# Optimization experiments

Hardware: AMD Instinct MI355X
Metric: run time of the kernel (lower is better)

Reference implementation:

```python
import jax, jax.numpy as jnp
import numpy as np

B, T, D_IN, H, D_OUT = 4096, 512, 10, 20, 2


def setup_inputs() -> dict:
    key = jax.random.key(0)
    ks = jax.random.split(key, 12)
    s = 1.0 / np.sqrt(H)  # PyTorch-style uniform bound scale (use normal*s)
    return {
        "x": jax.random.normal(ks[0], (B, T, D_IN), jnp.float32),
        "w_ih0": jax.random.normal(ks[1], (H, D_IN), jnp.float32) * s,
        "w_hh0": jax.random.normal(ks[2], (H, H), jnp.float32) * s,
        "b_ih0": jax.random.normal(ks[3], (H,), jnp.float32) * s,
        "b_hh0": jax.random.normal(ks[4], (H,), jnp.float32) * s,
        "w_ih1": jax.random.normal(ks[5], (H, H), jnp.float32) * s,
        "w_hh1": jax.random.normal(ks[6], (H, H), jnp.float32) * s,
        "b_ih1": jax.random.normal(ks[7], (H,), jnp.float32) * s,
        "b_hh1": jax.random.normal(ks[8], (H,), jnp.float32) * s,
        "fc_w": jax.random.normal(ks[9], (D_OUT, H), jnp.float32) * s,
        "fc_b": jax.random.normal(ks[10], (D_OUT,), jnp.float32) * s,
    }


def _rnn_layer(inp, w_ih, w_hh, b_ih, b_hh):
    # inp: [B, T, Din]. Precompute input projection once (batched GEMM),
    # then scan the sequential recurrence: h_t = tanh(x_t W_ih^T + b_ih + h_{t-1} W_hh^T + b_hh)
    xp = jnp.einsum('btd,hd->bth', inp, w_ih) + (b_ih + b_hh)  # [B, T, H]

    def step(h, xt):
        h = jnp.tanh(xt + h @ w_hh.T)
        return h, h

    h0 = jnp.zeros((inp.shape[0], w_hh.shape[0]), inp.dtype)
    _, hs = jax.lax.scan(step, h0, jnp.swapaxes(xp, 0, 1))  # hs: [T, B, H]
    return jnp.swapaxes(hs, 0, 1)  # [B, T, H]


def reference(x, w_ih0, w_hh0, b_ih0, b_hh0, w_ih1, w_hh1, b_ih1, b_hh1, fc_w, fc_b):
    h1 = _rnn_layer(x, w_ih0, w_hh0, b_ih0, b_hh0)
    h2 = _rnn_layer(h1, w_ih1, w_hh1, b_ih1, b_hh1)
    last = h2[:, -1, :]  # [B, H]
    return last @ fc_w.T + fc_b  # [B, D_OUT]
```

## Files before the change

### kernel.cpp

```cpp
#include <hip/hip_runtime.h>
#include <cstdint>

constexpr int B_   = 4096;
constexpr int T_   = 512;
constexpr int DIN  = 10;
constexpr int H_   = 20;
constexpr int DOUT = 2;

constexpr int SPW = 3;
constexpr int CH  = 4;
constexpr int XV  = CH * DIN / 4;

#define CFENCE() asm volatile("" ::: "memory")

__device__ __forceinline__ float fast_tanh(float v) {
    float e = __builtin_amdgcn_exp2f(v * 2.885390082f);
    float r = __builtin_amdgcn_rcpf(e + 1.0f);
    return fmaf(-2.0f, r, 1.0f);
}

extern "C" __global__ void __launch_bounds__(64, 1)
rnn_skew(const float* __restrict__ x,
         const float* __restrict__ w_ih0, const float* __restrict__ w_hh0,
         const float* __restrict__ b_ih0, const float* __restrict__ b_hh0,
         const float* __restrict__ w_ih1, const float* __restrict__ w_hh1,
         const float* __restrict__ b_ih1, const float* __restrict__ b_hh1,
         const float* __restrict__ fc_w, const float* __restrict__ fc_b,
         float* __restrict__ out)
{
    const int lane = threadIdx.x;
    const int sl   = lane / H_;
    const int i    = lane - sl * H_;
    const int samp = blockIdx.x * SPW + sl;
    const int sc   = (samp < B_) ? samp : (B_ - 1);
    const int slc  = (sl < SPW) ? sl : SPW;

    __shared__ __align__(16) float h1s[SPW + 1][H_];
    __shared__ __align__(16) float h2s[SPW + 1][H_];

    float wi0[DIN];
    {
        const float2* p = reinterpret_cast<const float2*>(w_ih0 + i * DIN);
        #pragma unroll
        for (int k = 0; k < DIN / 2; ++k) {
            float2 v = p[k];
            wi0[2 * k] = v.x; wi0[2 * k + 1] = v.y;
        }
    }
    float wh0[H_], wi1[H_], wh1[H_];
    {
        const float4* p0 = reinterpret_cast<const float4*>(w_hh0 + i * H_);
        const float4* p1 = reinterpret_cast<const float4*>(w_ih1 + i * H_);
        const float4* p2 = reinterpret_cast<const float4*>(w_hh1 + i * H_);
        #pragma unroll
        for (int k = 0; k < H_ / 4; ++k) {
            float4 a = p0[k]; wh0[4*k]=a.x; wh0[4*k+1]=a.y; wh0[4*k+2]=a.z; wh0[4*k+3]=a.w;
            float4 b = p1[k]; wi1[4*k]=b.x; wi1[4*k+1]=b.y; wi1[4*k+2]=b.z; wi1[4*k+3]=b.w;
            float4 c = p2[k]; wh1[4*k]=c.x; wh1[4*k+1]=c.y; wh1[4*k+2]=c.z; wh1[4*k+3]=c.w;
        }
    }
    const float bias0 = b_ih0[i] + b_hh0[i];
    const float bias1 = b_ih1[i] + b_hh1[i];

    float4 h1q[H_ / 4], h2q[H_ / 4];
    #pragma unroll
    for (int k = 0; k < H_ / 4; ++k) {
        h1q[k] = make_float4(0.f, 0.f, 0.f, 0.f);
        h2q[k] = make_float4(0.f, 0.f, 0.f, 0.f);
    }

    const float4* xb = reinterpret_cast<const float4*>(x + (size_t)sc * (T_ * DIN));

    float4 xv[XV];
    #pragma unroll
    for (int k = 0; k < XV; ++k) xv[k] = xb[k];

    auto full_step = [&](float xpm) {
        float a0 = xpm, a1 = 0.f, a2 = 0.f, a3 = 0.f;
        float b0 = bias1, b1 = 0.f, b2 = 0.f, b3 = 0.f;
        #pragma unroll
        for (int k = 0; k < H_ / 4; ++k) {
            a0 = fmaf(h1q[k].x, wh0[4*k+0], a0);
            a1 = fmaf(h1q[k].y, wh0[4*k+1], a1);
            a2 = fmaf(h1q[k].z, wh0[4*k+2], a2);
            a3 = fmaf(h1q[k].w, wh0[4*k+3], a3);
            b0 = fmaf(h1q[k].x, wi1[4*k+0], b0);
            b1 = fmaf(h1q[k].y, wi1[4*k+1], b1);
            b2 = fmaf(h1q[k].z, wi1[4*k+2], b2);
            b3 = fmaf(h1q[k].w, wi1[4*k+3], b3);
        }
        #pragma unroll
        for (int k = 0; k < H_ / 4; ++k) {
            b0 = fmaf(h2q[k].x, wh1[4*k+0], b0);
            b1 = fmaf(h2q[k].y, wh1[4*k+1], b1);
            b2 = fmaf(h2q[k].z, wh1[4*k+2], b2);
            b3 = fmaf(h2q[k].w, wh1[4*k+3], b3);
        }
        float h1n = fast_tanh((a0 + a1) + (a2 + a3));
        float h2n = fast_tanh((b0 + b1) + (b2 + b3));
        CFENCE();
        h1s[slc][i] = h1n;
        h2s[slc][i] = h2n;
        CFENCE();
        #pragma unroll
        for (int k = 0; k < H_ / 4; ++k)
            h1q[k] = reinterpret_cast<const float4*>(&h1s[slc][0])[k];
        #pragma unroll
        for (int k = 0; k < H_ / 4; ++k)
            h2q[k] = reinterpret_cast<const float4*>(&h2s[slc][0])[k];
        CFENCE();
    };

    auto consume_xp = [&](float* xp) {
        #pragma unroll
        for (int m = 0; m < CH; ++m) xp[m] = bias0;
        #pragma unroll
        for (int k = 0; k < XV; ++k) {
            int idx = 4 * k;
            xp[(idx+0)/DIN] = fmaf(xv[k].x, wi0[(idx+0)%DIN], xp[(idx+0)/DIN]);
            xp[(idx+1)/DIN] = fmaf(xv[k].y, wi0[(idx+1)%DIN], xp[(idx+1)/DIN]);
            xp[(idx+2)/DIN] = fmaf(xv[k].z, wi0[(idx+2)%DIN], xp[(idx+2)/DIN]);
            xp[(idx+3)/DIN] = fmaf(xv[k].w, wi0[(idx+3)%DIN], xp[(idx+3)/DIN]);
        }
    };

    {
        float xp[CH];
        consume_xp(xp);
        #pragma unroll
        for (int k = 0; k < XV; ++k) xv[k] = xb[(CH * DIN) / 4 + k];

        float h1n = fast_tanh(xp[0]);
        CFENCE();
        h1s[slc][i] = h1n;
        CFENCE();
        #pragma unroll
        for (int k = 0; k < H_ / 4; ++k)
            h1q[k] = reinterpret_cast<const float4*>(&h1s[slc][0])[k];
        CFENCE();

        #pragma unroll
        for (int m = 1; m < CH; ++m) full_step(xp[m]);
    }

    for (int t0 = CH; t0 < T_; t0 += CH) {
        float xp[CH];
        consume_xp(xp);
        {
            const int t0n = (t0 + CH < T_) ? (t0 + CH) : 0;
            #pragma unroll
            for (int k = 0; k < XV; ++k) xv[k] = xb[(t0n * DIN) / 4 + k];
        }
        #pragma unroll
        for (int m = 0; m < CH; ++m) full_step(xp[m]);
    }

    {
        float b0 = bias1, b1 = 0.f, b2 = 0.f, b3 = 0.f;
        #pragma unroll
        for (int k = 0; k < H_ / 4; ++k) {
            b0 = fmaf(h1q[k].x, wi1[4*k+0], b0);
            b1 = fmaf(h1q[k].y, wi1[4*k+1], b1);
            b2 = fmaf(h1q[k].z, wi1[4*k+2], b2);
            b3 = fmaf(h1q[k].w, wi1[4*k+3], b3);
        }
        #pragma unroll
        for (int k = 0; k < H_ / 4; ++k) {
            b0 = fmaf(h2q[k].x, wh1[4*k+0], b0);
            b1 = fmaf(h2q[k].y, wh1[4*k+1], b1);
            b2 = fmaf(h2q[k].z, wh1[4*k+2], b2);
            b3 = fmaf(h2q[k].w, wh1[4*k+3], b3);
        }
        float h2n = fast_tanh((b0 + b1) + (b2 + b3));
        CFENCE();
        h2s[slc][i] = h2n;
        CFENCE();
        #pragma unroll
        for (int k = 0; k < H_ / 4; ++k)
            h2q[k] = reinterpret_cast<const float4*>(&h2s[slc][0])[k];
        CFENCE();
    }

    if (sl < SPW && samp < B_ && i < DOUT) {
        float hf[H_];
        #pragma unroll
        for (int k = 0; k < H_ / 4; ++k) {
            hf[4*k+0] = h2q[k].x; hf[4*k+1] = h2q[k].y;
            hf[4*k+2] = h2q[k].z; hf[4*k+3] = h2q[k].w;
        }
        float acc = fc_b[i];
        #pragma unroll
        for (int j = 0; j < H_; ++j) acc = fmaf(hf[j], fc_w[i * H_ + j], acc);
        out[samp * DOUT + i] = acc;
    }
}

extern "C" void kernel_launch(void* const* d_in, const int* in_sizes, int n_in,
                              void* d_out, int out_size, void* d_ws, size_t ws_size,
                              hipStream_t stream) {
    (void)in_sizes; (void)n_in; (void)d_ws; (void)ws_size; (void)out_size;
    const float* x     = (const float*)d_in[0];
    const float* w_ih0 = (const float*)d_in[1];
    const float* w_hh0 = (const float*)d_in[2];
    const float* b_ih0 = (const float*)d_in[3];
    const float* b_hh0 = (const float*)d_in[4];
    const float* w_ih1 = (const float*)d_in[5];
    const float* w_hh1 = (const float*)d_in[6];
    const float* b_ih1 = (const float*)d_in[7];
    const float* b_hh1 = (const float*)d_in[8];
    const float* fc_w  = (const float*)d_in[9];
    const float* fc_b  = (const float*)d_in[10];
    float* out = (float*)d_out;

    const int grid = (B_ + SPW - 1) / SPW;
    hipLaunchKernelGGL(rnn_skew, dim3(grid), dim3(64), 0, stream,
                       x, w_ih0, w_hh0, b_ih0, b_hh0,
                       w_ih1, w_hh1, b_ih1, b_hh1, fc_w, fc_b, out);
}
```

Before: 154.3 us.

## Interleave two independent sample chains per lane to hide recurrence latency

Each 64-lane block now maps 2 samples per lane group (2 groups of 20 lanes) and runs two independent recurrences per lane, interleaving their compute and LDS exchange. The goal is ILP that hides the serial FMA/tanh/LDS latency of one chain behind the other. In exchange, 40 of 64 lanes are active instead of 60, there are fewer blocks (1024 vs 1366), register pressure roughly doubles, and the x chunk drops from 4 to 2 timesteps.

After: 242.3 us. 1.57x slower.

```diff
diff --git a/kernel.cpp b/kernel.cpp
--- a/kernel.cpp
+++ b/kernel.cpp
@@ -7,8 +7,9 @@
 constexpr int H_   = 20;
 constexpr int DOUT = 2;
 
-constexpr int SPW = 3;
-constexpr int CH  = 4;
+constexpr int SPW = 2;
+constexpr int NCH = 2;
+constexpr int CH  = 2;
 constexpr int XV  = CH * DIN / 4;
 
 #define CFENCE() asm volatile("" ::: "memory")
@@ -20,7 +21,7 @@
 }
 
 extern "C" __global__ void __launch_bounds__(64, 1)
-rnn_skew(const float* __restrict__ x,
+rnn_dual(const float* __restrict__ x,
          const float* __restrict__ w_ih0, const float* __restrict__ w_hh0,
          const float* __restrict__ b_ih0, const float* __restrict__ b_hh0,
          const float* __restrict__ w_ih1, const float* __restrict__ w_hh1,
@@ -31,12 +32,16 @@
     const int lane = threadIdx.x;
     const int sl   = lane / H_;
     const int i    = lane - sl * H_;
-    const int samp = blockIdx.x * SPW + sl;
-    const int sc   = (samp < B_) ? samp : (B_ - 1);
-    const int slc  = (sl < SPW) ? sl : SPW;
-
-    __shared__ __align__(16) float h1s[SPW + 1][H_];
-    __shared__ __align__(16) float h2s[SPW + 1][H_];
+    const bool act = (sl < SPW);
+    const int sampA = blockIdx.x * (SPW * NCH) + sl;
+    const int sampB = sampA + SPW;
+    const int scA = act ? min(sampA, B_ - 1) : (B_ - 1);
+    const int scB = act ? min(sampB, B_ - 1) : (B_ - 1);
+    const int rowA = act ? sl : 4;
+    const int rowB = act ? (SPW + sl) : 4;
+
+    __shared__ __align__(16) float h1s[2 * SPW + 1][H_];
+    __shared__ __align__(16) float h2s[2 * SPW + 1][H_];
 
     float wi0[DIN];
     {
@@ -62,20 +67,22 @@
     const float bias0 = b_ih0[i] + b_hh0[i];
     const float bias1 = b_ih1[i] + b_hh1[i];
 
-    float4 h1q[H_ / 4], h2q[H_ / 4];
+    float4 h1qA[H_/4], h2qA[H_/4], h1qB[H_/4], h2qB[H_/4];
     #pragma unroll
     for (int k = 0; k < H_ / 4; ++k) {
-        h1q[k] = make_float4(0.f, 0.f, 0.f, 0.f);
-        h2q[k] = make_float4(0.f, 0.f, 0.f, 0.f);
-    }
-
-    const float4* xb = reinterpret_cast<const float4*>(x + (size_t)sc * (T_ * DIN));
-
-    float4 xv[XV];
+        h1qA[k] = make_float4(0.f,0.f,0.f,0.f); h2qA[k] = make_float4(0.f,0.f,0.f,0.f);
+        h1qB[k] = make_float4(0.f,0.f,0.f,0.f); h2qB[k] = make_float4(0.f,0.f,0.f,0.f);
+    }
+
+    const float4* xbA = reinterpret_cast<const float4*>(x + (size_t)scA * (T_ * DIN));
+    const float4* xbB = reinterpret_cast<const float4*>(x + (size_t)scB * (T_ * DIN));
+
+    float4 xvA[XV], xvB[XV];
     #pragma unroll
-    for (int k = 0; k < XV; ++k) xv[k] = xb[k];
-
-    auto full_step = [&](float xpm) {
+    for (int k = 0; k < XV; ++k) { xvA[k] = xbA[k]; xvB[k] = xbB[k]; }
+
+    auto compute2 = [&](const float4 (&h1q)[H_/4], const float4 (&h2q)[H_/4],
+                        float xpm, float& h1n, float& h2n) {
         float a0 = xpm, a1 = 0.f, a2 = 0.f, a3 = 0.f;
         float b0 = bias1, b1 = 0.f, b2 = 0.f, b3 = 0.f;
         #pragma unroll
@@ -96,22 +103,36 @@
             b2 = fmaf(h2q[k].z, wh1[4*k+2], b2);
             b3 = fmaf(h2q[k].w, wh1[4*k+3], b3);
         }
-        float h1n = fast_tanh((a0 + a1) + (a2 + a3));
-        float h2n = fast_tanh((b0 + b1) + (b2 + b3));
-        CFENCE();
-        h1s[slc][i] = h1n;
-        h2s[slc][i] = h2n;
-        CFENCE();
+        h1n = fast_tanh((a0 + a1) + (a2 + a3));
+        h2n = fast_tanh((b0 + b1) + (b2 + b3));
+    };
+
+    auto readback = [&](float4 (&h1q)[H_/4], float4 (&h2q)[H_/4], int row) {
         #pragma unroll
         for (int k = 0; k < H_ / 4; ++k)
-            h1q[k] = reinterpret_cast<const float4*>(&h1s[slc][0])[k];
+            h1q[k] = reinterpret_cast<const float4*>(&h1s[row][0])[k];
         #pragma unroll
         for (int k = 0; k < H_ / 4; ++k)
-            h2q[k] = reinterpret_cast<const float4*>(&h2s[slc][0])[k];
-        CFENCE();
-    };
-
-    auto consume_xp = [&](float* xp) {
+            h2q[k] = reinterpret_cast<const float4*>(&h2s[row][0])[k];
+    };
+
+    auto step_pair = [&](float xpa, float xpb) {
+        float h1nA, h2nA, h1nB, h2nB;
+        compute2(h1qA, h2qA, xpa, h1nA, h2nA);
+        CFENCE();
+        h1s[rowA][i] = h1nA; h2s[rowA][i] = h2nA;
+        CFENCE();
+        compute2(h1qB, h2qB, xpb, h1nB, h2nB);
+        CFENCE();
+        h1s[rowB][i] = h1nB; h2s[rowB][i] = h2nB;
+        CFENCE();
+        readback(h1qA, h2qA, rowA);
+        CFENCE();
+        readback(h1qB, h2qB, rowB);
+        CFENCE();
+    };
+
+    auto consume_xp = [&](const float4 (&xv)[XV], float (&xp)[CH]) {
         #pragma unroll
         for (int m = 0; m < CH; ++m) xp[m] = bias0;
         #pragma unroll
@@ -125,73 +146,90 @@
     };
 
     {
-        float xp[CH];
-        consume_xp(xp);
-        #pragma unroll
-        for (int k = 0; k < XV; ++k) xv[k] = xb[(CH * DIN) / 4 + k];
-
-        float h1n = fast_tanh(xp[0]);
-        CFENCE();
-        h1s[slc][i] = h1n;
-        CFENCE();
-        #pragma unroll
-        for (int k = 0; k < H_ / 4; ++k)
-            h1q[k] = reinterpret_cast<const float4*>(&h1s[slc][0])[k];
-        CFENCE();
-
-        #pragma unroll
-        for (int m = 1; m < CH; ++m) full_step(xp[m]);
+        float xpA[CH], xpB[CH];
+        consume_xp(xvA, xpA);
+        consume_xp(xvB, xpB);
+        #pragma unroll
+        for (int k = 0; k < XV; ++k) {
+            xvA[k] = xbA[(CH * DIN) / 4 + k];
+            xvB[k] = xbB[(CH * DIN) / 4 + k];
+        }
+        float h1nA = fast_tanh(xpA[0]);
+        float h1nB = fast_tanh(xpB[0]);
+        CFENCE();
+        h1s[rowA][i] = h1nA; h1s[rowB][i] = h1nB;
+        CFENCE();
+        #pragma unroll
+        for (int k = 0; k < H_ / 4; ++k) {
+            h1qA[k] = reinterpret_cast<const float4*>(&h1s[rowA][0])[k];
+            h1qB[k] = reinterpret_cast<const float4*>(&h1s[rowB][0])[k];
+        }
+        CFENCE();
+        #pragma unroll
+        for (int m = 1; m < CH; ++m) step_pair(xpA[m], xpB[m]);
     }
 
     for (int t0 = CH; t0 < T_; t0 += CH) {
-        float xp[CH];
-        consume_xp(xp);
+        float xpA[CH], xpB[CH];
+        consume_xp(xvA, xpA);
+        consume_xp(xvB, xpB);
         {
             const int t0n = (t0 + CH < T_) ? (t0 + CH) : 0;
+            const int base = t0n * DIN / 4;
             #pragma unroll
-            for (int k = 0; k < XV; ++k) xv[k] = xb[(t0n * DIN) / 4 + k];
-        }
-        #pragma unroll
-        for (int m = 0; m < CH; ++m) full_step(xp[m]);
-    }
-
-    {
-        float b0 = bias1, b1 = 0.f, b2 = 0.f, b3 = 0.f;
-        #pragma unroll
-        for (int k = 0; k < H_ / 4; ++k) {
-            b0 = fmaf(h1q[k].x, wi1[4*k+0], b0);
-            b1 = fmaf(h1q[k].y, wi1[4*k+1], b1);
-            b2 = fmaf(h1q[k].z, wi1[4*k+2], b2);
-            b3 = fmaf(h1q[k].w, wi1[4*k+3], b3);
-        }
-        #pragma unroll
-        for (int k = 0; k < H_ / 4; ++k) {
-            b0 = fmaf(h2q[k].x, wh1[4*k+0], b0);
-            b1 = fmaf(h2q[k].y, wh1[4*k+1], b1);
-            b2 = fmaf(h2q[k].z, wh1[4*k+2], b2);
-            b3 = fmaf(h2q[k].w, wh1[4*k+3], b3);
-        }
-        float h2n = fast_tanh((b0 + b1) + (b2 + b3));
-        CFENCE();
-        h2s[slc][i] = h2n;
-        CFENCE();
-        #pragma unroll
-        for (int k = 0; k < H_ / 4; ++k)
-            h2q[k] = reinterpret_cast<const float4*>(&h2s[slc][0])[k];
-        CFENCE();
-    }
-
-    if (sl < SPW && samp < B_ && i < DOUT) {
-        float hf[H_];
-        #pragma unroll
-        for (int k = 0; k < H_ / 4; ++k) {
-            hf[4*k+0] = h2q[k].x; hf[4*k+1] = h2q[k].y;
-            hf[4*k+2] = h2q[k].z; hf[4*k+3] = h2q[k].w;
-        }
-        float acc = fc_b[i];
-        #pragma unroll
-        for (int j = 0; j < H_; ++j) acc = fmaf(hf[j], fc_w[i * H_ + j], acc);
-        out[samp * DOUT + i] = acc;
+            for (int k = 0; k < XV; ++k) { xvA[k] = xbA[base + k]; xvB[k] = xbB[base + k]; }
+        }
+        #pragma unroll
+        for (int m = 0; m < CH; ++m) step_pair(xpA[m], xpB[m]);
+    }
+
+    {
+        auto fin = [&](const float4 (&h1q)[H_/4], const float4 (&h2q)[H_/4]) -> float {
+            float b0 = bias1, b1 = 0.f, b2 = 0.f, b3 = 0.f;
+            #pragma unroll
+            for (int k = 0; k < H_ / 4; ++k) {
+                b0 = fmaf(h1q[k].x, wi1[4*k+0], b0);
+                b1 = fmaf(h1q[k].y, wi1[4*k+1], b1);
+                b2 = fmaf(h1q[k].z, wi1[4*k+2], b2);
+                b3 = fmaf(h1q[k].w, wi1[4*k+3], b3);
+            }
+            #pragma unroll
+            for (int k = 0; k < H_ / 4; ++k) {
+                b0 = fmaf(h2q[k].x, wh1[4*k+0], b0);
+                b1 = fmaf(h2q[k].y, wh1[4*k+1], b1);
+                b2 = fmaf(h2q[k].z, wh1[4*k+2], b2);
+                b3 = fmaf(h2q[k].w, wh1[4*k+3], b3);
+            }
+            return fast_tanh((b0 + b1) + (b2 + b3));
+        };
+        float h2nA = fin(h1qA, h2qA);
+        float h2nB = fin(h1qB, h2qB);
+        CFENCE();
+        h2s[rowA][i] = h2nA; h2s[rowB][i] = h2nB;
+        CFENCE();
+        #pragma unroll
+        for (int k = 0; k < H_ / 4; ++k) {
+            h2qA[k] = reinterpret_cast<const float4*>(&h2s[rowA][0])[k];
+            h2qB[k] = reinterpret_cast<const float4*>(&h2s[rowB][0])[k];
+        }
+        CFENCE();
+    }
+
+    if (act && i < DOUT) {
+        float accA = fc_b[i], accB = fc_b[i];
+        #pragma unroll
+        for (int k = 0; k < H_ / 4; ++k) {
+            accA = fmaf(h2qA[k].x, fc_w[i*H_ + 4*k+0], accA);
+            accA = fmaf(h2qA[k].y, fc_w[i*H_ + 4*k+1], accA);
+            accA = fmaf(h2qA[k].z, fc_w[i*H_ + 4*k+2], accA);
+            accA = fmaf(h2qA[k].w, fc_w[i*H_ + 4*k+3], accA);
+            accB = fmaf(h2qB[k].x, fc_w[i*H_ + 4*k+0], accB);
+            accB = fmaf(h2qB[k].y, fc_w[i*H_ + 4*k+1], accB);
+            accB = fmaf(h2qB[k].z, fc_w[i*H_ + 4*k+2], accB);
+            accB = fmaf(h2qB[k].w, fc_w[i*H_ + 4*k+3], accB);
+        }
+        if (sampA < B_) out[sampA * DOUT + i] = accA;
+        if (sampB < B_) out[sampB * DOUT + i] = accB;
     }
 }
 
@@ -212,8 +250,8 @@
     const float* fc_b  = (const float*)d_in[10];
     float* out = (float*)d_out;
 
-    const int grid = (B_ + SPW - 1) / SPW;
-    hipLaunchKernelGGL(rnn_skew, dim3(grid), dim3(64), 0, stream,
+    const int grid = B_ / (SPW * NCH);
+    hipLaunchKernelGGL(rnn_dual, dim3(grid), dim3(64), 0, stream,
                        x, w_ih0, w_hh0, b_ih0, b_hh0,
                        w_ih1, w_hh1, b_ih1, b_hh1, fc_w, fc_b, out);
 }
```
